# Optimization experiments

Hardware: AMD Instinct MI355X
Metric: run time of the kernel (lower is better)

## Reference

```python
import jax, jax.numpy as jnp
import numpy as np

B, NB, L, H, C = 4, 256, 64, 8, 128
N = NB * L
D = C // H
EG_HID = 16


def setup_inputs() -> dict:
    key = jax.random.key(0)
    ks = jax.random.split(key, 10)
    x = jax.random.normal(ks[0], (B, N, C), jnp.float32)
    attn_mask = jax.random.randint(ks[1], (B, NB, L, L), 0, 2, jnp.int32)
    edge_feats = jax.random.normal(ks[2], (B, NB, L, L, 4), jnp.float32)
    # learned params (torch Linear convention: y = x @ W.T + b)
    qkv_w = jax.random.normal(ks[3], (3 * C, C), jnp.float32) * 0.02
    qkv_b = jnp.zeros((3 * C,), jnp.float32)
    proj_w = jax.random.normal(ks[4], (C, C), jnp.float32) * 0.02
    proj_b = jnp.zeros((C,), jnp.float32)
    eg_w1 = jax.random.normal(ks[5], (EG_HID, 4), jnp.float32) * 0.01
    eg_b1 = jnp.zeros((EG_HID,), jnp.float32)
    eg_w2 = jax.random.normal(ks[6], (H, EG_HID), jnp.float32) * 0.01
    eg_b2 = jnp.zeros((H,), jnp.float32)
    return {"x": x, "attn_mask": attn_mask, "edge_feats": edge_feats,
            "qkv_w": qkv_w, "qkv_b": qkv_b, "proj_w": proj_w, "proj_b": proj_b,
            "eg_w1": eg_w1, "eg_b1": eg_b1, "eg_w2": eg_w2, "eg_b2": eg_b2}


def reference(x, attn_mask, edge_feats, qkv_w, qkv_b, proj_w, proj_b, eg_w1, eg_b1, eg_w2, eg_b2):
    Bx, Nx, Cx = x.shape
    nb = Nx // L                     # N divisible by L -> no padding branch
    scale = D ** -0.5
    dt = x.dtype

    xb = x.reshape(Bx, nb, L, Cx)    # (B, nb, L, C)
    eye = jnp.eye(L, dtype=bool)

    # mask: force self-attention where a query row has no neighbors
    mask = attn_mask.astype(dt)                       # (B, nb, L, L)
    need = (mask.sum(axis=-1) < 1).astype(dt)         # (B, nb, L)
    mask = jnp.where(eye, jnp.maximum(mask, need[..., None]), mask)

    # bias_physics: zero the diagonal, set channel 3 on the diagonal to 1
    bias = edge_feats * (~eye)[..., None].astype(dt)  # (B, nb, L, L, 4)
    bias = bias + eye[..., None].astype(dt) * jnp.array([0.0, 0.0, 0.0, 1.0], dt)

    # qkv projection
    qkv = xb @ qkv_w.T + qkv_b                        # (B, nb, L, 3C)
    q, k, v = jnp.split(qkv, 3, axis=-1)
    q = q.reshape(Bx, nb, L, H, D).transpose(0, 1, 3, 2, 4)  # (B, nb, H, L, D)
    k = k.reshape(Bx, nb, L, H, D).transpose(0, 1, 3, 2, 4)
    v = v.reshape(Bx, nb, L, H, D).transpose(0, 1, 3, 2, 4)

    # edge-gated per-head bias: small MLP over 4 edge features, gated by mask
    hgate = jax.nn.gelu(bias @ eg_w1.T + eg_b1, approximate=False)  # (B, nb, L, L, 16)
    eg = (hgate @ eg_w2.T + eg_b2) * mask[..., None]                # (B, nb, L, L, H)
    eg = jnp.moveaxis(eg, -1, 2)                                    # (B, nb, H, L, L)

    logit_bias = bias[..., 3]                                       # (B, nb, L, L)

    scores = jnp.einsum('bnhqd,bnhkd->bnhqk', q, k) * scale
    scores = scores + logit_bias[:, :, None] + eg
    scores = jnp.where((mask > 0)[:, :, None], scores, jnp.asarray(-1e9, dt))
    attn = jax.nn.softmax(scores, axis=-1)

    out = jnp.einsum('bnhqk,bnhkd->bnhqd', attn, v)                 # (B, nb, H, L, D)
    out = out.transpose(0, 1, 3, 2, 4).reshape(Bx, Nx, Cx)
    return out @ proj_w.T + proj_b
```

## Files before the change

### kernel.cpp

```cpp
#include <hip/hip_runtime.h>

typedef _Float16 f16x2 __attribute__((ext_vector_type(2)));
typedef _Float16 f16x4 __attribute__((ext_vector_type(4)));
typedef _Float16 f16x8 __attribute__((ext_vector_type(8)));
typedef float    f32x4  __attribute__((ext_vector_type(4)));
typedef float    f32x16 __attribute__((ext_vector_type(16)));

#define MFMA32(a, b, c) __builtin_amdgcn_mfma_f32_32x32x16_f16((a), (b), (c), 0, 0, 0)
#define MFMA16(a, b, c) __builtin_amdgcn_mfma_f32_16x16x32_f16((a), (b), (c), 0, 0, 0)

__device__ __forceinline__ int swz(int row, int col) {
    return (row * 128 + col) ^ ((row & 7) << 3);
}
__device__ __forceinline__ int vswz(int d, int tok) {
    return d * 64 + (tok ^ ((d & 7) << 3));
}

__device__ __forceinline__ float dot2f(f16x2 a, f16x2 b, float c) {
#if __has_builtin(__builtin_amdgcn_fdot2)
    return __builtin_amdgcn_fdot2(a, b, c, false);
#else
    return c + (float)a[0] * (float)b[0] + (float)a[1] * (float)b[1];
#endif
}
__device__ __forceinline__ f16x2 mkh2(float a, float b) {
    f16x2 r; r[0] = (_Float16)a; r[1] = (_Float16)b; return r;
}
__device__ __forceinline__ f16x2 dup2(float v) {
    _Float16 h = (_Float16)v; f16x2 r; r[0] = h; r[1] = h; return r;
}
__device__ __forceinline__ unsigned packh(float a, float b) {
    union { f16x2 h; unsigned u; } c; c.h = mkh2(a, b); return c.u;
}
__device__ __forceinline__ f16x8 cvt8(float4 a, float4 b) {
    f16x8 r;
    r[0] = (_Float16)a.x; r[1] = (_Float16)a.y; r[2] = (_Float16)a.z; r[3] = (_Float16)a.w;
    r[4] = (_Float16)b.x; r[5] = (_Float16)b.y; r[6] = (_Float16)b.z; r[7] = (_Float16)b.w;
    return r;
}
__device__ __forceinline__ f16x4 cvt4(float4 a) {
    f16x4 r;
    r[0] = (_Float16)a.x; r[1] = (_Float16)a.y; r[2] = (_Float16)a.z; r[3] = (_Float16)a.w;
    return r;
}

__global__ __launch_bounds__(512) void pack_w(
    const float* __restrict__ qkv_w, const float* __restrict__ proj_w,
    _Float16* __restrict__ wfrag)
{
    const int f = blockIdx.x * 512 + threadIdx.x;
    const int seg = f >> 12, r = f & 4095;
    const int wv = r >> 9, ks = (r >> 6) & 7, lane = r & 63;
    const int l31 = lane & 31, hi = lane >> 5;
    const float* src;
    if (seg == 0) {
        const int qk = wv >> 2, m0 = (wv & 3) * 32;
        src = qkv_w + (size_t)(qk * 128 + m0 + l31) * 128 + ks * 16 + hi * 8;
    } else if (seg == 1) {
        const int n0v = (wv >> 1) * 32;
        src = qkv_w + (size_t)(256 + n0v + l31) * 128 + ks * 16 + hi * 8;
    } else {
        const int n0 = (wv >> 1) * 32;
        src = proj_w + (size_t)(n0 + l31) * 128 + ks * 16 + hi * 8;
    }
    float4 a = *(const float4*)src, b = *(const float4*)(src + 4);
    *(f16x8*)&wfrag[(size_t)f * 8] = cvt8(a, b);
}

struct __align__(16) SmemF {
    union { _Float16 xb[64 * 128]; _Float16 ao[64 * 128]; };
    union { _Float16 QK[2][64 * 128]; _Float16 Pc[8][64 * 40]; };
    _Float16 Vt[128 * 64];
    float    inv[8 * 64];
    unsigned wpk[112];
};

template <bool PACKED>
__global__ __launch_bounds__(512, 4) void fused_all(
    const float* __restrict__ x, const int* __restrict__ am, const float* __restrict__ ef,
    const float* __restrict__ qkv_w, const float* __restrict__ qkv_b,
    const float* __restrict__ proj_w, const float* __restrict__ proj_b,
    const float* __restrict__ w1, const float* __restrict__ b1,
    const float* __restrict__ w2, const float* __restrict__ b2,
    const _Float16* __restrict__ wfrag,
    _Float16* __restrict__ egw,
    float* __restrict__ out)
{
    __shared__ SmemF sm;
    const int t    = threadIdx.x;
    const int lane = t & 63;
    const int w    = __builtin_amdgcn_readfirstlane(t >> 6);
    const int bid  = blockIdx.x;
    const int l31  = lane & 31, hi = lane >> 5;
    const int l15  = lane & 15, g4 = lane >> 4;
    const int qrow = t >> 3,  k8 = t & 7;

    {
        const float4* __restrict__ xp = (const float4*)(x + (size_t)bid * 8192);
        #pragma unroll
        for (int i = 0; i < 4; ++i) {
            int f = t + i * 512;
            float4 v = xp[f];
            int row = f >> 5, c0 = (f & 31) * 4;
            *(f16x4*)&sm.xb[swz(row, c0 & ~7) + (c0 & 7)] = cvt4(v);
        }
        if (t < 112) {
            unsigned v;
            if (t < 32)       { int f = t >> 3, jp = t & 7;
                                v = packh(w1[2 * jp * 4 + f], w1[(2 * jp + 1) * 4 + f]); }
            else if (t < 40)  { int jp = t - 32; v = packh(b1[2 * jp], b1[2 * jp + 1]); }
            else if (t < 104) { int i = t - 40, h = i >> 3, jp = i & 7;
                                v = packh(w2[h * 16 + 2 * jp], w2[h * 16 + 2 * jp + 1]); }
            else              { v = __float_as_uint(b2[t - 104]); }
            sm.wpk[t] = v;
        }
    }
    __syncthreads();

    auto MLP = [&]() {
        const size_t pb = (size_t)bid * 4096;
        const int* amr = am + pb + (size_t)qrow * 64 + k8 * 8;
        int4 ma = *(const int4*)amr, mb = *(const int4*)(amr + 4);
        int rs = ma.x + ma.y + ma.z + ma.w + mb.x + mb.y + mb.z + mb.w;
        rs += __shfl_xor(rs, 1); rs += __shfl_xor(rs, 2); rs += __shfl_xor(rs, 4);
        const int need = (rs < 1) ? 1 : 0;
        const float4* __restrict__ efr = (const float4*)ef + pb + (size_t)qrow * 64 + k8 * 8;

        const f16x2* __restrict__ wp2 = (const f16x2*)sm.wpk;
        f16x2 w1p[4][8], b1p[8];
        #pragma unroll
        for (int f = 0; f < 4; ++f)
            #pragma unroll
            for (int jp = 0; jp < 8; ++jp) w1p[f][jp] = wp2[f * 8 + jp];
        #pragma unroll
        for (int jp = 0; jp < 8; ++jp) b1p[jp] = wp2[32 + jp];

        const f16x2 C3 = dup2(-0.002976190476f), C2 = dup2(0.025f), C1 = dup2(-0.16666667f);
        const f16x2 ONE = dup2(1.0f), HALF = dup2(0.5f), RH = dup2(0.39894228040f);

        int mk[8] = {ma.x, ma.y, ma.z, ma.w, mb.x, mb.y, mb.z, mb.w};
        float lbv[8];
        f16x2 hg[8][8];
        #pragma unroll
        for (int j = 0; j < 8; ++j) {
            float4 e = efr[j];
            int m = mk[j];
            if (k8 * 8 + j == qrow) { e.x = 0.f; e.y = 0.f; e.z = 0.f; e.w = 1.f; m = (m > need) ? m : need; }
            mk[j] = m; lbv[j] = e.w;
            f16x2 ex = dup2(e.x), ey = dup2(e.y), ez = dup2(e.z), ew = dup2(e.w);
            #pragma unroll
            for (int jp = 0; jp < 8; ++jp) {
                f16x2 a = b1p[jp];
                a = ex * w1p[0][jp] + a;
                a = ey * w1p[1][jp] + a;
                a = ez * w1p[2][jp] + a;
                a = ew * w1p[3][jp] + a;
                f16x2 u  = a * a;
                f16x2 p  = u * C3 + C2;
                p        = p * u + C1;
                p        = p * u + ONE;
                f16x2 rx = a * RH;
                f16x2 g  = rx * p + HALF;
                hg[j][jp] = a * g;
            }
        }
        _Float16* base = egw + (size_t)bid * 32768 + (size_t)qrow * 64 + k8 * 8;
        #pragma unroll
        for (int h = 0; h < 8; ++h) {
            f16x2 w2p[8];
            #pragma unroll
            for (int jp = 0; jp < 8; ++jp) w2p[jp] = wp2[40 + h * 8 + jp];
            const float b2v = __uint_as_float(sm.wpk[104 + h]);
            f16x8 o8;
            #pragma unroll
            for (int j = 0; j < 8; ++j) {
                float acc = b2v;
                #pragma unroll
                for (int jp = 0; jp < 8; ++jp) acc = dot2f(hg[j][jp], w2p[jp], acc);
                float vv = acc + lbv[j];
                o8[j] = (mk[j] > 0) ? (_Float16)vv : (_Float16)(-30000.0f);
            }
            *(f16x8*)&base[h * 4096] = o8;
        }
    };

    auto QKV = [&]() {
        const int qk = w >> 2;
        const int m0 = (w & 3) * 32;
        f16x8 afr[8];
        if (PACKED) {
            const f16x8* __restrict__ wa = (const f16x8*)wfrag + (size_t)(w * 8) * 64 + lane;
            #pragma unroll
            for (int ks = 0; ks < 8; ++ks) afr[ks] = wa[ks * 64];
        } else {
            const float4* __restrict__ wb4 =
                (const float4*)(qkv_w + (size_t)(qk * 128 + m0 + l31) * 128) + hi * 2;
            #pragma unroll
            for (int ks = 0; ks < 8; ++ks) {
                float4 wa = wb4[ks * 4], wbv = wb4[ks * 4 + 1];
                afr[ks] = cvt8(wa, wbv);
            }
        }
        f32x16 acc0 = {0,0,0,0,0,0,0,0,0,0,0,0,0,0,0,0};
        f32x16 acc1 = {0,0,0,0,0,0,0,0,0,0,0,0,0,0,0,0};
        #pragma unroll
        for (int ks = 0; ks < 8; ++ks) {
            f16x8 b0  = *(const f16x8*)&sm.xb[swz(l31,      ks * 16 + hi * 8)];
            f16x8 b1v = *(const f16x8*)&sm.xb[swz(32 + l31, ks * 16 + hi * 8)];
            acc0 = MFMA32(afr[ks], b0, acc0);
            acc1 = MFMA32(afr[ks], b1v, acc1);
        }
        const float qs = qk ? 1.0f : 0.25f;
        _Float16* dst = sm.QK[qk];
        #pragma unroll
        for (int g2 = 0; g2 < 4; ++g2) {
            const int d = m0 + 8 * g2 + 4 * hi;
            f16x4 pa, pb;
            #pragma unroll
            for (int j = 0; j < 4; ++j) {
                float bz = qkv_b[qk * 128 + d + j];
                pa[j] = (_Float16)((acc0[4 * g2 + j] + bz) * qs);
                pb[j] = (_Float16)((acc1[4 * g2 + j] + bz) * qs);
            }
            *(f16x4*)&dst[swz(l31,      d)] = pa;
            *(f16x4*)&dst[swz(32 + l31, d)] = pb;
        }
        const int mt0 = (w & 1) * 32, n0v = (w >> 1) * 32;
        f16x8 vfr[8];
        if (PACKED) {
            const f16x8* __restrict__ wv = (const f16x8*)wfrag + 4096 + (size_t)(w * 8) * 64 + lane;
            #pragma unroll
            for (int ks = 0; ks < 8; ++ks) vfr[ks] = wv[ks * 64];
        } else {
            const float4* __restrict__ vb4 =
                (const float4*)(qkv_w + (size_t)(256 + n0v + l31) * 128) + hi * 2;
            #pragma unroll
            for (int ks = 0; ks < 8; ++ks) {
                float4 wa = vb4[ks * 4], wbv = vb4[ks * 4 + 1];
                vfr[ks] = cvt8(wa, wbv);
            }
        }
        f32x16 accv = {0,0,0,0,0,0,0,0,0,0,0,0,0,0,0,0};
        #pragma unroll
        for (int ks = 0; ks < 8; ++ks) {
            f16x8 a = *(const f16x8*)&sm.xb[swz(mt0 + l31, ks * 16 + hi * 8)];
            accv = MFMA32(a, vfr[ks], accv);
        }
        const float vbias = qkv_b[256 + n0v + l31];
        #pragma unroll
        for (int g2 = 0; g2 < 4; ++g2) {
            f16x4 pk;
            #pragma unroll
            for (int j = 0; j < 4; ++j) pk[j] = (_Float16)(accv[4 * g2 + j] + vbias);
            *(f16x4*)&sm.Vt[vswz(n0v + l31, mt0 + 8 * g2 + 4 * hi)] = pk;
        }
    };

    f16x4 egf[2][2][4];
    auto EGF = [&]() {
        const _Float16* egb = egw + (size_t)bid * 32768 + (size_t)w * 4096 + l31 * 64 + hi * 4;
        #pragma unroll
        for (int ni = 0; ni < 2; ++ni)
            #pragma unroll
            for (int mi = 0; mi < 2; ++mi)
                #pragma unroll
                for (int g2 = 0; g2 < 4; ++g2)
                    egf[ni][mi][g2] = *(const f16x4*)&egb[ni * 2048 + mi * 32 + g2 * 8];
    };

    if ((bid & 1) == 0) {
        MLP();
        __syncthreads();
        EGF();
        QKV();
    } else {
        QKV();
        __syncthreads();
        MLP();
    }
    __syncthreads();
    if (bid & 1) EGF();

    const int h = w;
    f32x16 S0n0, S0n1, S1n0, S1n1;
    {
        const int dcol = h * 16 + hi * 8;
        f16x8 ka0 = *(const f16x8*)&sm.QK[1][swz(l31,      dcol)];
        f16x8 ka1 = *(const f16x8*)&sm.QK[1][swz(32 + l31, dcol)];
        f16x8 qb0 = *(const f16x8*)&sm.QK[0][swz(l31,      dcol)];
        f16x8 qb1 = *(const f16x8*)&sm.QK[0][swz(32 + l31, dcol)];
        f32x16 z = {0,0,0,0,0,0,0,0,0,0,0,0,0,0,0,0};
        S0n0 = MFMA32(ka0, qb0, z); S0n1 = MFMA32(ka0, qb1, z);
        S1n0 = MFMA32(ka1, qb0, z); S1n1 = MFMA32(ka1, qb1, z);
    }
    {
        auto sfx = [&](f32x16& Sa, f32x16& Sb, int ni, int q) {
            #pragma unroll
            for (int g2 = 0; g2 < 4; ++g2) {
                #pragma unroll
                for (int j = 0; j < 4; ++j) {
                    Sa[4 * g2 + j] += (float)egf[ni][0][g2][j];
                    Sb[4 * g2 + j] += (float)egf[ni][1][g2][j];
                }
            }
            float mx = -__builtin_inff();
            #pragma unroll
            for (int r = 0; r < 16; ++r) mx = fmaxf(mx, fmaxf(Sa[r], Sb[r]));
            mx = fmaxf(mx, __shfl_xor(mx, 32));
            float sum = 0.f;
            #pragma unroll
            for (int r = 0; r < 16; ++r) {
                Sa[r] = __expf(Sa[r] - mx); sum += Sa[r];
                Sb[r] = __expf(Sb[r] - mx); sum += Sb[r];
            }
            sum += __shfl_xor(sum, 32);
            if (hi == 0) sm.inv[h * 64 + q] = 1.0f / sum;
        };
        sfx(S0n0, S1n0, 0, l31);
        sfx(S0n1, S1n1, 1, 32 + l31);
    }
    __syncthreads();

    f16x8 pfr[8];
    if (PACKED) {
        const f16x8* __restrict__ wp = (const f16x8*)wfrag + 8192 + (size_t)(w * 8) * 64 + lane;
        #pragma unroll
        for (int ks = 0; ks < 8; ++ks) pfr[ks] = wp[ks * 64];
    } else {
        const int n0 = (w >> 1) * 32;
        const float4* __restrict__ pb4 =
            (const float4*)(proj_w + (size_t)(n0 + l31) * 128) + hi * 2;
        #pragma unroll
        for (int ks = 0; ks < 8; ++ks) {
            float4 wa = pb4[ks * 4], wbv = pb4[ks * 4 + 1];
            pfr[ks] = cvt8(wa, wbv);
        }
    }
    {
        f32x4 o0 = {0,0,0,0}, o1 = {0,0,0,0}, o2 = {0,0,0,0}, o3 = {0,0,0,0};
        _Float16* pc = sm.Pc[h];
        auto chunk = [&](const f32x16& Pn0, const f32x16& Pn1, int c) {
            #pragma unroll
            for (int g2 = 0; g2 < 4; ++g2) {
                const int ko = 8 * g2 + 4 * hi;
                f16x4 a, bq;
                #pragma unroll
                for (int j = 0; j < 4; ++j) {
                    a[j]  = (_Float16)Pn0[4 * g2 + j];
                    bq[j] = (_Float16)Pn1[4 * g2 + j];
                }
                *(f16x4*)&pc[l31 * 40 + ko]        = a;
                *(f16x4*)&pc[(32 + l31) * 40 + ko] = bq;
            }
            f16x8 av = *(const f16x8*)&sm.Vt[vswz(h * 16 + l15, c * 32 + g4 * 8)];
            f16x8 p0 = *(const f16x8*)&pc[(l15) * 40 + g4 * 8];
            f16x8 p1 = *(const f16x8*)&pc[(16 + l15) * 40 + g4 * 8];
            f16x8 p2 = *(const f16x8*)&pc[(32 + l15) * 40 + g4 * 8];
            f16x8 p3 = *(const f16x8*)&pc[(48 + l15) * 40 + g4 * 8];
            o0 = MFMA16(av, p0, o0); o1 = MFMA16(av, p1, o1);
            o2 = MFMA16(av, p2, o2); o3 = MFMA16(av, p3, o3);
        };
        chunk(S0n0, S0n1, 0);
        chunk(S1n0, S1n1, 1);

        const int d0 = g4 * 4;
        float iv0 = sm.inv[h * 64 +  0 + l15];
        float iv1 = sm.inv[h * 64 + 16 + l15];
        float iv2 = sm.inv[h * 64 + 32 + l15];
        float iv3 = sm.inv[h * 64 + 48 + l15];
        f16x4 w0, w1v, w2v, w3;
        #pragma unroll
        for (int j = 0; j < 4; ++j) {
            w0[j]  = (_Float16)(o0[j] * iv0);
            w1v[j] = (_Float16)(o1[j] * iv1);
            w2v[j] = (_Float16)(o2[j] * iv2);
            w3[j]  = (_Float16)(o3[j] * iv3);
        }
        *(f16x4*)&sm.ao[swz( 0 + l15, h * 16 + d0)] = w0;
        *(f16x4*)&sm.ao[swz(16 + l15, h * 16 + d0)] = w1v;
        *(f16x4*)&sm.ao[swz(32 + l15, h * 16 + d0)] = w2v;
        *(f16x4*)&sm.ao[swz(48 + l15, h * 16 + d0)] = w3;
    }
    __syncthreads();

    {
        const int m0 = (w & 1) * 32, n0 = (w >> 1) * 32;
        f32x16 acc = {0,0,0,0,0,0,0,0,0,0,0,0,0,0,0,0};
        #pragma unroll
        for (int ks = 0; ks < 8; ++ks) {
            f16x8 a = *(const f16x8*)&sm.ao[swz(m0 + l31, ks * 16 + hi * 8)];
            acc = MFMA32(a, pfr[ks], acc);
        }
        const float bias = proj_b[n0 + l31];
        float* op = out + (size_t)bid * 8192 + n0 + l31;
        #pragma unroll
        for (int r = 0; r < 16; ++r) {
            const int tok = m0 + (r & 3) + 8 * (r >> 2) + 4 * hi;
            op[tok * 128] = acc[r] + bias;
        }
    }
}

extern "C" void kernel_launch(void* const* d_in, const int* in_sizes, int n_in,
                              void* d_out, int out_size, void* d_ws, size_t ws_size,
                              hipStream_t stream) {
    (void)in_sizes; (void)n_in; (void)out_size;
    const float* x      = (const float*)d_in[0];
    const int*   am     = (const int*)d_in[1];
    const float* ef     = (const float*)d_in[2];
    const float* qkv_w  = (const float*)d_in[3];
    const float* qkv_b  = (const float*)d_in[4];
    const float* proj_w = (const float*)d_in[5];
    const float* proj_b = (const float*)d_in[6];
    const float* w1     = (const float*)d_in[7];
    const float* b1     = (const float*)d_in[8];
    const float* w2     = (const float*)d_in[9];
    const float* b2     = (const float*)d_in[10];

    const size_t eg_bytes = (size_t)1024 * 32768 * sizeof(_Float16);
    const size_t wf_off   = 262144;
    if (ws_size >= wf_off + eg_bytes) {
        _Float16* wfrag = (_Float16*)d_ws;
        _Float16* egw   = (_Float16*)((char*)d_ws + wf_off);
        pack_w<<<dim3(24), dim3(512), 0, stream>>>(qkv_w, proj_w, wfrag);
        fused_all<true><<<dim3(1024), dim3(512), 0, stream>>>(
            x, am, ef, qkv_w, qkv_b, proj_w, proj_b, w1, b1, w2, b2,
            wfrag, egw, (float*)d_out);
    } else {
        fused_all<false><<<dim3(1024), dim3(512), 0, stream>>>(
            x, am, ef, qkv_w, qkv_b, proj_w, proj_b, w1, b1, w2, b2,
            (const _Float16*)d_ws, (_Float16*)d_ws, (float*)d_out);
    }
}
```

Baseline: 76.00 us.

## Transpose edge-gate bias through shared memory instead of a global workspace round-trip

Each block used to write its per-head edge-gate bias (64 MB fp16 across the grid) to a global workspace and read it back in MFMA fragment layout. It now stages the bias through a new shared-memory transpose buffer, unioned with the QK/P region, in two passes of four heads. Each pass is followed by barriers so the owning waves can load their fragments. This removes the global write/read traffic and the odd/even block ordering of MLP and QKV, at the cost of extra barriers and losing the overlap that ordering gave.

After: 64.82 us. -14.7%, faster.

```diff
diff --git a/kernel.cpp b/kernel.cpp
--- a/kernel.cpp
+++ b/kernel.cpp
@@ -69,8 +69,10 @@
 
 struct __align__(16) SmemF {
     union { _Float16 xb[64 * 128]; _Float16 ao[64 * 128]; };
-    union { _Float16 QK[2][64 * 128]; _Float16 Pc[8][64 * 40]; };
-    _Float16 Vt[128 * 64];
+    union { _Float16 QK[2][64 * 128];
+            _Float16 Pc[8][64 * 40];
+            _Float16 tb[4 * 4224]; };
+    union { _Float16 Vt[128 * 64]; };
     float    inv[8 * 64];
     unsigned wpk[112];
 };
@@ -83,7 +85,6 @@
     const float* __restrict__ w1, const float* __restrict__ b1,
     const float* __restrict__ w2, const float* __restrict__ b2,
     const _Float16* __restrict__ wfrag,
-    _Float16* __restrict__ egw,
     float* __restrict__ out)
 {
     __shared__ SmemF sm;
@@ -117,7 +118,10 @@
     }
     __syncthreads();
 
-    auto MLP = [&]() {
+    int mk[8];
+    float lbv[8];
+    f16x2 hg[8][8];
+    {
         const size_t pb = (size_t)bid * 4096;
         const int* amr = am + pb + (size_t)qrow * 64 + k8 * 8;
         int4 ma = *(const int4*)amr, mb = *(const int4*)(amr + 4);
@@ -138,9 +142,8 @@
         const f16x2 C3 = dup2(-0.002976190476f), C2 = dup2(0.025f), C1 = dup2(-0.16666667f);
         const f16x2 ONE = dup2(1.0f), HALF = dup2(0.5f), RH = dup2(0.39894228040f);
 
-        int mk[8] = {ma.x, ma.y, ma.z, ma.w, mb.x, mb.y, mb.z, mb.w};
-        float lbv[8];
-        f16x2 hg[8][8];
+        mk[0] = ma.x; mk[1] = ma.y; mk[2] = ma.z; mk[3] = ma.w;
+        mk[4] = mb.x; mk[5] = mb.y; mk[6] = mb.z; mk[7] = mb.w;
         #pragma unroll
         for (int j = 0; j < 8; ++j) {
             float4 e = efr[j];
@@ -164,27 +167,55 @@
                 hg[j][jp] = a * g;
             }
         }
-        _Float16* base = egw + (size_t)bid * 32768 + (size_t)qrow * 64 + k8 * 8;
-        #pragma unroll
-        for (int h = 0; h < 8; ++h) {
-            f16x2 w2p[8];
-            #pragma unroll
-            for (int jp = 0; jp < 8; ++jp) w2p[jp] = wp2[40 + h * 8 + jp];
-            const float b2v = __uint_as_float(sm.wpk[104 + h]);
-            f16x8 o8;
-            #pragma unroll
-            for (int j = 0; j < 8; ++j) {
-                float acc = b2v;
+    }
+
+    f16x4 egf[2][2][4];
+    {
+        const f16x2* __restrict__ wp2 = (const f16x2*)sm.wpk;
+        const int ni = qrow >> 5, q31 = qrow & 31;
+        const int segi = (ni * 2 + (k8 >> 2)) * 4 + (k8 & 3);
+        _Float16* tbase = sm.tb;
+
+        #pragma unroll 1
+        for (int r = 0; r < 2; ++r) {
+            #pragma unroll
+            for (int h2 = 0; h2 < 4; ++h2) {
+                const int h = r * 4 + h2;
+                f16x2 w2p[8];
                 #pragma unroll
-                for (int jp = 0; jp < 8; ++jp) acc = dot2f(hg[j][jp], w2p[jp], acc);
-                float vv = acc + lbv[j];
-                o8[j] = (mk[j] > 0) ? (_Float16)vv : (_Float16)(-30000.0f);
-            }
-            *(f16x8*)&base[h * 4096] = o8;
-        }
-    };
-
-    auto QKV = [&]() {
+                for (int jp = 0; jp < 8; ++jp) w2p[jp] = wp2[40 + h * 8 + jp];
+                const float b2v = __uint_as_float(sm.wpk[104 + h]);
+                f16x4 lo4, hi4;
+                #pragma unroll
+                for (int j = 0; j < 8; ++j) {
+                    float acc = b2v;
+                    #pragma unroll
+                    for (int jp = 0; jp < 8; ++jp) acc = dot2f(hg[j][jp], w2p[jp], acc);
+                    float vv = acc + lbv[j];
+                    _Float16 ov = (mk[j] > 0) ? (_Float16)vv : (_Float16)(-30000.0f);
+                    if (j < 4) lo4[j] = ov; else hi4[j - 4] = ov;
+                }
+                *(f16x4*)&tbase[h2 * 4224 + segi * 264 + q31 * 4]       = lo4;
+                *(f16x4*)&tbase[h2 * 4224 + segi * 264 + 128 + q31 * 4] = hi4;
+            }
+            __syncthreads();
+            if ((w >> 2) == r) {
+                const int h2 = w & 3;
+                const int hk = lane >> 5, ql = lane & 31;
+                #pragma unroll
+                for (int ni2 = 0; ni2 < 2; ++ni2)
+                    #pragma unroll
+                    for (int mi = 0; mi < 2; ++mi)
+                        #pragma unroll
+                        for (int g2 = 0; g2 < 4; ++g2)
+                            egf[ni2][mi][g2] = *(const f16x4*)
+                                &tbase[h2 * 4224 + ((ni2 * 2 + mi) * 4 + g2) * 264 + hk * 128 + ql * 4];
+            }
+            __syncthreads();
+        }
+    }
+
+    {
         const int qk = w >> 2;
         const int m0 = (w & 3) * 32;
         f16x8 afr[8];
@@ -254,32 +285,8 @@
             for (int j = 0; j < 4; ++j) pk[j] = (_Float16)(accv[4 * g2 + j] + vbias);
             *(f16x4*)&sm.Vt[vswz(n0v + l31, mt0 + 8 * g2 + 4 * hi)] = pk;
         }
-    };
-
-    f16x4 egf[2][2][4];
-    auto EGF = [&]() {
-        const _Float16* egb = egw + (size_t)bid * 32768 + (size_t)w * 4096 + l31 * 64 + hi * 4;
-        #pragma unroll
-        for (int ni = 0; ni < 2; ++ni)
-            #pragma unroll
-            for (int mi = 0; mi < 2; ++mi)
-                #pragma unroll
-                for (int g2 = 0; g2 < 4; ++g2)
-                    egf[ni][mi][g2] = *(const f16x4*)&egb[ni * 2048 + mi * 32 + g2 * 8];
-    };
-
-    if ((bid & 1) == 0) {
-        MLP();
-        __syncthreads();
-        EGF();
-        QKV();
-    } else {
-        QKV();
-        __syncthreads();
-        MLP();
     }
     __syncthreads();
-    if (bid & 1) EGF();
 
     const int h = w;
     f32x16 S0n0, S0n1, S1n0, S1n1;
@@ -417,18 +424,16 @@
     const float* w2     = (const float*)d_in[9];
     const float* b2     = (const float*)d_in[10];
 
-    const size_t eg_bytes = (size_t)1024 * 32768 * sizeof(_Float16);
-    const size_t wf_off   = 262144;
-    if (ws_size >= wf_off + eg_bytes) {
+    const size_t wf_bytes = 196608;
+    if (ws_size >= wf_bytes) {
         _Float16* wfrag = (_Float16*)d_ws;
-        _Float16* egw   = (_Float16*)((char*)d_ws + wf_off);
         pack_w<<<dim3(24), dim3(512), 0, stream>>>(qkv_w, proj_w, wfrag);
         fused_all<true><<<dim3(1024), dim3(512), 0, stream>>>(
             x, am, ef, qkv_w, qkv_b, proj_w, proj_b, w1, b1, w2, b2,
-            wfrag, egw, (float*)d_out);
+            wfrag, (float*)d_out);
     } else {
         fused_all<false><<<dim3(1024), dim3(512), 0, stream>>>(
             x, am, ef, qkv_w, qkv_b, proj_w, proj_b, w1, b1, w2, b2,
-            (const _Float16*)d_ws, (_Float16*)d_ws, (float*)d_out);
-    }
-}
+            (const _Float16*)nullptr, (float*)d_out);
+    }
+}
```
